# Kernel tuning notes

Hardware: AMD Instinct MI355X
Metric: run time of the kernel (lower is better)

Reference implementation:

```python
import jax, jax.numpy as jnp
import numpy as np

N = 100000
E = 3200000
F_IN = 128
H1 = 16
H2 = 8
NEG_SLOPE = 0.2


def _gat_layer(x, src, dst, W, a_src, a_dst, b, n_nodes):
    # x: [N, Fin]; src/dst: [E_tot] (self-loops included); W: [Fin, Fout]
    h = x @ W                                   # [N, Fout]
    e_src = h @ a_src                           # [N]
    e_dst = h @ a_dst                           # [N]
    e = e_src[src] + e_dst[dst]                 # [E_tot]
    e = jnp.where(e > 0, e, NEG_SLOPE * e)      # leaky_relu(0.2)
    m = jax.ops.segment_max(e, dst, num_segments=n_nodes)   # [N]
    w = jnp.exp(e - m[dst])                     # [E_tot]
    s = jax.ops.segment_sum(w, dst, num_segments=n_nodes)   # [N]
    alpha = w / s[dst]                          # [E_tot]
    out = jax.ops.segment_sum(alpha[:, None] * h[src], dst, num_segments=n_nodes)
    return out + b


def setup_inputs() -> dict:
    key = jax.random.key(0)
    ks = jax.random.split(key, 12)
    x = jax.random.normal(ks[0], (N, F_IN), dtype=jnp.float32)
    edge_index = jax.random.randint(ks[1], (E, 2), 0, N, dtype=jnp.int64)
    s1 = 1.0 / np.sqrt(F_IN)
    s2 = 1.0 / np.sqrt(H1)
    s3 = 1.0 / np.sqrt(H2)
    return {
        "x": x,
        "edge_index": edge_index,
        "W1": jax.random.normal(ks[2], (F_IN, H1), dtype=jnp.float32) * s1,
        "a1_src": jax.random.normal(ks[3], (H1,), dtype=jnp.float32) * s2,
        "a1_dst": jax.random.normal(ks[4], (H1,), dtype=jnp.float32) * s2,
        "b1": jnp.zeros((H1,), dtype=jnp.float32),
        "W2": jax.random.normal(ks[5], (H1, H2), dtype=jnp.float32) * s2,
        "a2_src": jax.random.normal(ks[6], (H2,), dtype=jnp.float32) * s3,
        "a2_dst": jax.random.normal(ks[7], (H2,), dtype=jnp.float32) * s3,
        "b2": jnp.zeros((H2,), dtype=jnp.float32),
        "Wf": jax.random.normal(ks[8], (H2, 1), dtype=jnp.float32) * s3,
        "bf": jnp.zeros((1,), dtype=jnp.float32),
    }


def reference(x, edge_index, W1, a1_src, a1_dst, b1, W2, a2_src, a2_dst, b2, Wf, bf):
    ei = edge_index.T                            # [2, E] as in original forward
    loop = jnp.arange(N, dtype=ei.dtype)
    src = jnp.concatenate([ei[0], loop])         # PyG add_self_loops=True
    dst = jnp.concatenate([ei[1], loop])
    h = jax.nn.relu(_gat_layer(x, src, dst, W1, a1_src, a1_dst, b1, N))
    # dropout p=0.05 is identity at inference
    h = jax.nn.relu(_gat_layer(h, src, dst, W2, a2_src, a2_dst, b2, N))
    return h @ Wf + bf                           # [N, 1]
```

## Files before the change

### kernel.cpp

```cpp
#include <hip/hip_runtime.h>
#include <math.h>

#define N_NODES 100000
#define N_EDGES 3200000
#define E_TOT   (N_EDGES + N_NODES)
#define F_IN    128
#define H1      16
#define H2      8
#define NEG     0.2f
#define NBUCKET ((N_NODES + 255) >> 8)
#define NCHUNK  512
#define CE      ((N_EDGES + NCHUNK - 1) / NCHUNK)

typedef _Float16 half2v __attribute__((ext_vector_type(2)));
typedef _Float16 half8v __attribute__((ext_vector_type(8)));

__global__ __launch_bounds__(256) void k1_xw(
        const float* __restrict__ x, const float* __restrict__ W1,
        const float* __restrict__ a1s, const float* __restrict__ a1d,
        char* __restrict__ g1, float* __restrict__ e1d) {
    __shared__ float w1s[F_IN * H1];
    __shared__ float xs[16 * 132];
    __shared__ float a1ss[H1], a1ds[H1];
    const int tid = threadIdx.x;
    for (int i = tid; i < F_IN * H1; i += 256) w1s[i] = W1[i];
    if (tid < H1) { a1ss[tid] = a1s[tid]; a1ds[tid] = a1d[tid]; }
    const int rowbase = blockIdx.x * 16;
    #pragma unroll
    for (int i = 0; i < 2; i++) {
        int q = tid + i * 256;
        int r = q >> 5, c = q & 31;
        float4 v = *(const float4*)(x + (size_t)(rowbase + r) * F_IN + c * 4);
        *(float4*)(xs + r * 132 + c * 4) = v;
    }
    __syncthreads();
    const int g = tid >> 4, j = tid & 15;
    const float* xrow = xs + g * 132;
    float acc = 0.f;
    #pragma unroll 8
    for (int k = 0; k < F_IN; k++) acc += xrow[k] * w1s[k * H1 + j];
    const int row = rowbase + g;
    char* grow = g1 + (size_t)row * 64;
    ((_Float16*)grow)[j] = (_Float16)acc;
    float ps = acc * a1ss[j];
    float pd = acc * a1ds[j];
    #pragma unroll
    for (int m = 8; m >= 1; m >>= 1) {
        ps += __shfl_xor(ps, m, 16);
        pd += __shfl_xor(pd, m, 16);
    }
    if (j == 0) { *(float*)(grow + 32) = ps; e1d[row] = pd; }
}


__global__ __launch_bounds__(256) void k_count(const int2* __restrict__ ei,
                                               int* __restrict__ counts) {
    __shared__ int hist[NBUCKET];
    for (int i = threadIdx.x; i < NBUCKET; i += 256) hist[i] = 0;
    __syncthreads();
    const int b = blockIdx.x;
    const int beg = b * CE, end = min(N_EDGES, beg + CE);
    for (int e = beg + threadIdx.x; e < end; e += 256)
        atomicAdd(&hist[ei[e].y >> 8], 1);
    __syncthreads();
    for (int i = threadIdx.x; i < NBUCKET; i += 256)
        counts[i * NCHUNK + b] = hist[i];
}

__global__ __launch_bounds__(512) void k_scanA(int* __restrict__ counts,
                                               int* __restrict__ btot) {
    __shared__ int lds[NCHUNK];
    const int k = blockIdx.x, t = threadIdx.x;
    int v = counts[k * NCHUNK + t];
    lds[t] = v;
    __syncthreads();
    for (int off = 1; off < NCHUNK; off <<= 1) {
        int u = (t >= off) ? lds[t - off] : 0;
        __syncthreads();
        lds[t] += u;
        __syncthreads();
    }
    counts[k * NCHUNK + t] = lds[t] - v;
    if (t == NCHUNK - 1) btot[k] = lds[t];
}

__global__ __launch_bounds__(512) void k_scanB(const int* __restrict__ btot,
                                               int* __restrict__ bbase) {
    __shared__ int lds[512];
    const int t = threadIdx.x;
    int v = (t < NBUCKET) ? btot[t] : 0;
    lds[t] = v;
    __syncthreads();
    for (int off = 1; off < 512; off <<= 1) {
        int u = (t >= off) ? lds[t - off] : 0;
        __syncthreads();
        lds[t] += u;
        __syncthreads();
    }
    if (t < NBUCKET) bbase[t] = lds[t] - v;
    if (t == 511) bbase[NBUCKET] = lds[511];
}

__global__ __launch_bounds__(256) void k_reorder(const int2* __restrict__ ei,
                                                 const int* __restrict__ counts,
                                                 const int* __restrict__ bbase,
                                                 int* __restrict__ pairs) {
    __shared__ int cur[NBUCKET];
    const int b = blockIdx.x;
    for (int i = threadIdx.x; i < NBUCKET; i += 256)
        cur[i] = bbase[i] + counts[i * NCHUNK + b];
    __syncthreads();
    const int beg = b * CE, end = min(N_EDGES, beg + CE);
    for (int e = beg + threadIdx.x; e < end; e += 256) {
        int2 v = ei[e];
        int k = v.y >> 8;
        int pos = atomicAdd(&cur[k], 1);
        pairs[pos] = (v.x << 8) | (v.y & 255);
    }
}

__global__ __launch_bounds__(256) void k_csr(const int* __restrict__ pairs,
                                             const int* __restrict__ bbase,
                                             int* __restrict__ rowg,
                                             int* __restrict__ degg,
                                             int* __restrict__ sorted_src) {
    __shared__ int deg[256], scn[256], cur[256];
    const int k = blockIdx.x, t = threadIdx.x;
    const int n0 = k << 8;
    const int nn = min(256, N_NODES - n0);
    deg[t] = 0;
    __syncthreads();
    const int ebeg = bbase[k], eend = bbase[k + 1];
    for (int e = ebeg + t; e < eend; e += 256)
        atomicAdd(&deg[pairs[e] & 255], 1);
    __syncthreads();
    int v = (t < nn) ? deg[t] : 0;
    scn[t] = v;
    __syncthreads();
    for (int off = 1; off < 256; off <<= 1) {
        int u = (t >= off) ? scn[t - off] : 0;
        __syncthreads();
        scn[t] += u;
        __syncthreads();
    }
    int excl = scn[t] - v;
    if (t < nn) {
        int r = ebeg + excl + n0 + t;
        rowg[n0 + t] = r;
        degg[n0 + t] = v + 1;
        sorted_src[r] = n0 + t;
        cur[t] = r + 1;
    }
    __syncthreads();
    for (int e = ebeg + t; e < eend; e += 256) {
        int p = pairs[e];
        int pos = atomicAdd(&cur[p & 255], 1);
        sorted_src[pos] = p >> 8;
    }
}

template <int LPN, int U, int ROWB, int ESOFF, bool LAYER2>
__global__ __launch_bounds__(256) void k_agg(
        const int* __restrict__ row, const int* __restrict__ deg,
        const int* __restrict__ sorted_src,
        const float* __restrict__ ed, const char* __restrict__ gtab,
        const float* __restrict__ b,
        const float* __restrict__ W2, const float* __restrict__ a2s,
        const float* __restrict__ a2d,
        char* __restrict__ g2out, float* __restrict__ e2d_out,
        const float* __restrict__ Wf, const float* __restrict__ bf,
        float* __restrict__ out) {
    __shared__ float w2s[H1 * H2];
    __shared__ float a2ss[H2], a2ds[H2];
    if (!LAYER2) {
        for (int i = threadIdx.x; i < H1 * H2; i += 256) w2s[i] = W2[i];
        if (threadIdx.x < H2) { a2ss[threadIdx.x] = a2s[threadIdx.x];
                                a2ds[threadIdx.x] = a2d[threadIdx.x]; }
        __syncthreads();
    }
    const int sub = threadIdx.x & (LPN - 1);
    const int node = (blockIdx.x * 256 + threadIdx.x) / LPN;
    if (node >= N_NODES) return;
    const int beg = row[node];
    const int cnt = deg[node];
    const float edv = ed[node];
    float2 acc = make_float2(0.f, 0.f);
    float s = 0.f;
    int srcs[U];
    #pragma unroll
    for (int i = 0; i < U; i++) srcs[i] = sorted_src[beg + (i < cnt ? i : 0)];
    for (int t0 = 0; t0 < cnt; t0 += U) {
        float evs[U];
        half2v hvs[U];
        #pragma unroll
        for (int i = 0; i < U; i++) {
            const char* rp = gtab + (unsigned)srcs[i] * ROWB;
            hvs[i] = *(const half2v*)(rp + sub * 4);
            evs[i] = *(const float*)(rp + ESOFF);
        }
        int nsrcs[U];
        #pragma unroll
        for (int i = 0; i < U; i++) {
            int idx = t0 + U + i;
            nsrcs[i] = sorted_src[beg + (idx < cnt ? idx : 0)];
        }
        #pragma unroll
        for (int i = 0; i < U; i++) {
            if (t0 + i < cnt) {
                float e = evs[i] + edv;
                e = e > 0.f ? e : NEG * e;
                float p = __expf(e);
                s += p;
                acc.x += p * (float)hvs[i].x;
                acc.y += p * (float)hvs[i].y;
            }
        }
        #pragma unroll
        for (int i = 0; i < U; i++) srcs[i] = nsrcs[i];
    }
    const float inv = 1.f / s;
    const float2 bv = ((const float2*)b)[sub];
    float2 o;
    o.x = fmaxf(acc.x * inv + bv.x, 0.f);
    o.y = fmaxf(acc.y * inv + bv.y, 0.f);
    if (!LAYER2) {
        float p2[H2];
        const float* w0 = w2s + (2 * sub) * H2;
        const float* w1 = w2s + (2 * sub + 1) * H2;
        #pragma unroll
        for (int i = 0; i < H2; i++) p2[i] = o.x * w0[i] + o.y * w1[i];
        #pragma unroll
        for (int i = 0; i < H2; i++) {
            p2[i] += __shfl_xor(p2[i], 1);
            p2[i] += __shfl_xor(p2[i], 2);
            p2[i] += __shfl_xor(p2[i], 4);
        }
        float es2 = 0.f, ed2 = 0.f;
        #pragma unroll
        for (int i = 0; i < H2; i++) { es2 += p2[i] * a2ss[i]; ed2 += p2[i] * a2ds[i]; }
        char* orow = g2out + (size_t)node * 32;
        if (sub == 0) {
            half8v h8;
            #pragma unroll
            for (int i = 0; i < H2; i++) h8[i] = (_Float16)p2[i];
            *(half8v*)orow = h8;
        } else if (sub == 1) {
            *(float*)(orow + 16) = es2;
        } else if (sub == 2) {
            e2d_out[node] = ed2;
        }
    } else {
        const float2 wv = ((const float2*)Wf)[sub];
        float r = o.x * wv.x + o.y * wv.y;
        r += __shfl_xor(r, 1);
        r += __shfl_xor(r, 2);
        if (sub == 0) out[node] = r + bf[0];
    }
}

extern "C" void kernel_launch(void* const* d_in, const int* in_sizes, int n_in,
                              void* d_out, int out_size, void* d_ws, size_t ws_size,
                              hipStream_t stream) {
    const float* x    = (const float*)d_in[0];
    const int2*  ei   = (const int2*)d_in[1];
    const float* W1   = (const float*)d_in[2];
    const float* a1s  = (const float*)d_in[3];
    const float* a1d  = (const float*)d_in[4];
    const float* b1   = (const float*)d_in[5];
    const float* W2   = (const float*)d_in[6];
    const float* a2s  = (const float*)d_in[7];
    const float* a2d  = (const float*)d_in[8];
    const float* b2   = (const float*)d_in[9];
    const float* Wf   = (const float*)d_in[10];
    const float* bf   = (const float*)d_in[11];
    float* out = (float*)d_out;

    char* wp = (char*)d_ws;
    int* sorted_src = (int*)wp;   wp += sizeof(int) * (size_t)E_TOT;
    char* pairs_region = wp;      wp += sizeof(int) * (size_t)N_EDGES;
    int* counts     = (int*)wp;   wp += sizeof(int) * (size_t)NBUCKET * NCHUNK;
    int* btot       = (int*)wp;   wp += sizeof(int) * (NBUCKET + 1);
    int* bbase      = (int*)wp;   wp += sizeof(int) * (NBUCKET + 1);
    int* degg       = (int*)wp;   wp += sizeof(int) * N_NODES;
    int* rowg       = (int*)wp;   wp += sizeof(int) * N_NODES;

    int*   pairs = (int*)pairs_region;
    char*  g1    = pairs_region;
    char*  g2    = pairs_region + (size_t)64 * N_NODES;
    float* e1d   = (float*)(g2 + (size_t)32 * N_NODES);
    float* e2d   = e1d + N_NODES;

    k_count<<<NCHUNK, 256, 0, stream>>>(ei, counts);
    k_scanA<<<NBUCKET, 512, 0, stream>>>(counts, btot);
    k_scanB<<<1, 512, 0, stream>>>(btot, bbase);
    k_reorder<<<NCHUNK, 256, 0, stream>>>(ei, counts, bbase, pairs);
    k_csr<<<NBUCKET, 256, 0, stream>>>(pairs, bbase, rowg, degg, sorted_src);
    k1_xw<<<N_NODES / 16, 256, 0, stream>>>(x, W1, a1s, a1d, g1, e1d);
    k_agg<8, 8, 64, 32, false><<<(N_NODES * 8 + 255) / 256, 256, 0, stream>>>(
        rowg, degg, sorted_src, e1d, g1, b1, W2, a2s, a2d, g2, e2d,
        nullptr, nullptr, nullptr);
    k_agg<4, 8, 32, 16, true><<<(N_NODES * 4 + 255) / 256, 256, 0, stream>>>(
        rowg, degg, sorted_src, e2d, g2, b2, nullptr, nullptr, nullptr,
        nullptr, nullptr, Wf, bf, out);
}
```

Measured before the change: 269.3 us.

## Split source scores into separate arrays, compact feature rows, use exp2 with prescaled logits

Moves the per-node source attention score out of the padded gather rows into its own dense array, shrinking layer-1 rows from 64 to 32 bytes and layer-2 rows from 32 to 16. The logits are pre-multiplied by log2(e) so the aggregation can call the hardware exp2 directly, and leaky-relu becomes a fmax. Loads of the sorted source index stream are marked nontemporal. Each edge now does two random gathers (feature row and score) instead of one, so the smaller, denser tables must outweigh the extra memory requests.

```diff
diff --git a/kernel.cpp b/kernel.cpp
--- a/kernel.cpp
+++ b/kernel.cpp
@@ -8,6 +8,7 @@
 #define H1      16
 #define H2      8
 #define NEG     0.2f
+#define LOG2E   1.4426950408889634f
 #define NBUCKET ((N_NODES + 255) >> 8)
 #define NCHUNK  512
 #define CE      ((N_EDGES + NCHUNK - 1) / NCHUNK)
@@ -18,7 +19,7 @@
 __global__ __launch_bounds__(256) void k1_xw(
         const float* __restrict__ x, const float* __restrict__ W1,
         const float* __restrict__ a1s, const float* __restrict__ a1d,
-        char* __restrict__ g1, float* __restrict__ e1d) {
+        char* __restrict__ g1, float* __restrict__ es1, float* __restrict__ e1d) {
     __shared__ float w1s[F_IN * H1];
     __shared__ float xs[16 * 132];
     __shared__ float a1ss[H1], a1ds[H1];
@@ -40,8 +41,7 @@
     #pragma unroll 8
     for (int k = 0; k < F_IN; k++) acc += xrow[k] * w1s[k * H1 + j];
     const int row = rowbase + g;
-    char* grow = g1 + (size_t)row * 64;
-    ((_Float16*)grow)[j] = (_Float16)acc;
+    ((_Float16*)(g1 + (size_t)row * 32))[j] = (_Float16)acc;
     float ps = acc * a1ss[j];
     float pd = acc * a1ds[j];
     #pragma unroll
@@ -49,7 +49,7 @@
         ps += __shfl_xor(ps, m, 16);
         pd += __shfl_xor(pd, m, 16);
     }
-    if (j == 0) { *(float*)(grow + 32) = ps; e1d[row] = pd; }
+    if (j == 0) { es1[row] = ps * LOG2E; e1d[row] = pd * LOG2E; }
 }
 
 
@@ -159,15 +159,16 @@
     }
 }
 
-template <int LPN, int U, int ROWB, int ESOFF, bool LAYER2>
+template <int LPN, int U, int ROWB, bool LAYER2>
 __global__ __launch_bounds__(256) void k_agg(
         const int* __restrict__ row, const int* __restrict__ deg,
         const int* __restrict__ sorted_src,
-        const float* __restrict__ ed, const char* __restrict__ gtab,
-        const float* __restrict__ b,
+        const float* __restrict__ es, const float* __restrict__ ed,
+        const char* __restrict__ gtab, const float* __restrict__ b,
         const float* __restrict__ W2, const float* __restrict__ a2s,
         const float* __restrict__ a2d,
-        char* __restrict__ g2out, float* __restrict__ e2d_out,
+        char* __restrict__ g2out, float* __restrict__ es2_out,
+        float* __restrict__ e2d_out,
         const float* __restrict__ Wf, const float* __restrict__ bf,
         float* __restrict__ out) {
     __shared__ float w2s[H1 * H2];
@@ -188,7 +189,8 @@
     float s = 0.f;
     int srcs[U];
     #pragma unroll
-    for (int i = 0; i < U; i++) srcs[i] = sorted_src[beg + (i < cnt ? i : 0)];
+    for (int i = 0; i < U; i++)
+        srcs[i] = __builtin_nontemporal_load(sorted_src + beg + (i < cnt ? i : 0));
     for (int t0 = 0; t0 < cnt; t0 += U) {
         float evs[U];
         half2v hvs[U];
@@ -196,20 +198,20 @@
         for (int i = 0; i < U; i++) {
             const char* rp = gtab + (unsigned)srcs[i] * ROWB;
             hvs[i] = *(const half2v*)(rp + sub * 4);
-            evs[i] = *(const float*)(rp + ESOFF);
+            evs[i] = es[srcs[i]];
         }
         int nsrcs[U];
         #pragma unroll
         for (int i = 0; i < U; i++) {
             int idx = t0 + U + i;
-            nsrcs[i] = sorted_src[beg + (idx < cnt ? idx : 0)];
+            nsrcs[i] = __builtin_nontemporal_load(sorted_src + beg + (idx < cnt ? idx : 0));
         }
         #pragma unroll
         for (int i = 0; i < U; i++) {
             if (t0 + i < cnt) {
-                float e = evs[i] + edv;
-                e = e > 0.f ? e : NEG * e;
-                float p = __expf(e);
+                float k = evs[i] + edv;
+                k = fmaxf(k, NEG * k);
+                float p = __builtin_amdgcn_exp2f(k);
                 s += p;
                 acc.x += p * (float)hvs[i].x;
                 acc.y += p * (float)hvs[i].y;
@@ -238,16 +240,15 @@
         float es2 = 0.f, ed2 = 0.f;
         #pragma unroll
         for (int i = 0; i < H2; i++) { es2 += p2[i] * a2ss[i]; ed2 += p2[i] * a2ds[i]; }
-        char* orow = g2out + (size_t)node * 32;
         if (sub == 0) {
             half8v h8;
             #pragma unroll
             for (int i = 0; i < H2; i++) h8[i] = (_Float16)p2[i];
-            *(half8v*)orow = h8;
+            *(half8v*)(g2out + (size_t)node * 16) = h8;
         } else if (sub == 1) {
-            *(float*)(orow + 16) = es2;
+            es2_out[node] = es2 * LOG2E;
         } else if (sub == 2) {
-            e2d_out[node] = ed2;
+            e2d_out[node] = ed2 * LOG2E;
         }
     } else {
         const float2 wv = ((const float2*)Wf)[sub];
@@ -286,8 +287,10 @@
 
     int*   pairs = (int*)pairs_region;
     char*  g1    = pairs_region;
-    char*  g2    = pairs_region + (size_t)64 * N_NODES;
-    float* e1d   = (float*)(g2 + (size_t)32 * N_NODES);
+    char*  g2    = pairs_region + (size_t)32 * N_NODES;
+    float* es1   = (float*)(g2 + (size_t)16 * N_NODES);
+    float* es2   = es1 + N_NODES;
+    float* e1d   = es2 + N_NODES;
     float* e2d   = e1d + N_NODES;
 
     k_count<<<NCHUNK, 256, 0, stream>>>(ei, counts);
@@ -295,11 +298,11 @@
     k_scanB<<<1, 512, 0, stream>>>(btot, bbase);
     k_reorder<<<NCHUNK, 256, 0, stream>>>(ei, counts, bbase, pairs);
     k_csr<<<NBUCKET, 256, 0, stream>>>(pairs, bbase, rowg, degg, sorted_src);
-    k1_xw<<<N_NODES / 16, 256, 0, stream>>>(x, W1, a1s, a1d, g1, e1d);
-    k_agg<8, 8, 64, 32, false><<<(N_NODES * 8 + 255) / 256, 256, 0, stream>>>(
-        rowg, degg, sorted_src, e1d, g1, b1, W2, a2s, a2d, g2, e2d,
+    k1_xw<<<N_NODES / 16, 256, 0, stream>>>(x, W1, a1s, a1d, g1, es1, e1d);
+    k_agg<8, 8, 32, false><<<(N_NODES * 8 + 255) / 256, 256, 0, stream>>>(
+        rowg, degg, sorted_src, es1, e1d, g1, b1, W2, a2s, a2d, g2, es2, e2d,
         nullptr, nullptr, nullptr);
-    k_agg<4, 8, 32, 16, true><<<(N_NODES * 4 + 255) / 256, 256, 0, stream>>>(
-        rowg, degg, sorted_src, e2d, g2, b2, nullptr, nullptr, nullptr,
-        nullptr, nullptr, Wf, bf, out);
-}
+    k_agg<4, 8, 16, true><<<(N_NODES * 4 + 255) / 256, 256, 0, stream>>>(
+        rowg, degg, sorted_src, es2, e2d, g2, b2, nullptr, nullptr, nullptr,
+        nullptr, nullptr, nullptr, Wf, bf, out);
+}
```

Result: slower. 337.7 us (+25.4%).
